# Performance work log

Measured on AMD Instinct MI355X. Metric: run time of the kernel, lower is better.

The kernel has to match this reference:

```python
import jax, jax.numpy as jnp
import numpy as np

N_NODES = 100000
N_EDGES = 1000000
N_QUERY = 100000
F_IN = 64
HIDDEN = 64
LABEL_DIM = 2


def setup_inputs() -> dict:
    key = jax.random.key(0)
    ks = jax.random.split(key, 16)
    inp = {}
    for i, nm in enumerate(["Xr", "Xi", "Xj", "Xk"]):
        inp[nm] = jax.random.normal(ks[i], (N_NODES, F_IN), dtype=jnp.float32)
    for i, nm in enumerate(["norm_r", "norm_i", "norm_j", "norm_k"]):
        inp[nm] = jax.random.normal(ks[4 + i], (N_EDGES,), dtype=jnp.float32) * 0.1
    inp["edge_index"] = jax.random.randint(ks[8], (2, N_EDGES), 0, N_NODES)
    inp["query_edges"] = jax.random.randint(ks[9], (N_QUERY, 2), 0, N_NODES)
    s1 = (2.0 / (F_IN + HIDDEN)) ** 0.5  # glorot
    inp["W1"] = jax.random.normal(ks[10], (4, F_IN, HIDDEN), dtype=jnp.float32) * s1
    inp["b1"] = jnp.zeros((4, HIDDEN), dtype=jnp.float32)
    s2 = (2.0 / (HIDDEN + HIDDEN)) ** 0.5
    inp["W2"] = jax.random.normal(ks[11], (4, HIDDEN, HIDDEN), dtype=jnp.float32) * s2
    inp["b2"] = jnp.zeros((4, HIDDEN), dtype=jnp.float32)
    inp["Cw"] = jax.random.normal(ks[12], (LABEL_DIM, 8 * HIDDEN), dtype=jnp.float32) * 0.05
    inp["Cb"] = jnp.zeros((LABEL_DIM,), dtype=jnp.float32)
    return inp


def _quaconv(Xs, src, dst, norms, W, b, n_nodes):
    # Xs: list of 4 [N,F] components; norms: list of 4 [E] Laplacian norms.
    # P[a][b] = propagate(X_a, -norm_b) = scatter_add over dst of (-norm_b)_e * X_a[src_e]
    P = []
    for a in range(4):
        G = Xs[a][src]  # [E, F] gather, reused for all 4 norms
        P.append([jax.ops.segment_sum((-norms[b])[:, None] * G, dst, num_segments=n_nodes)
                  for b in range(4)])
    Tr = P[0][0] - P[1][1] - P[2][2] - P[3][3]
    Ti = P[1][0] + P[0][1] + P[3][2] - P[2][3]
    Tj = P[2][0] - P[3][1] + P[0][2] + P[1][3]
    Tk = P[3][0] + P[2][1] - P[1][2] + P[0][3]
    Wr, Wi, Wj, Wk = W[0], W[1], W[2], W[3]
    out_r = Tr @ Wr - Ti @ Wi - Tj @ Wj - Tk @ Wk + b[0]
    out_i = Tr @ Wi + Ti @ Wr + Tj @ Wk - Tk @ Wj + b[1]
    out_j = Tr @ Wj - Ti @ Wk + Tj @ Wr + Tk @ Wi + b[2]
    out_k = Tr @ Wk + Ti @ Wj - Tj @ Wi + Tk @ Wr + b[3]
    return out_r, out_i, out_j, out_k


def _forward(Xr, Xi, Xj, Xk, norm_r, norm_i, norm_j, norm_k,
             W1, b1, W2, b2, Cw, Cb, edge_index, query_edges):
    src, dst = edge_index[0], edge_index[1]
    n = Xr.shape[0]
    norms = [norm_r, norm_i, norm_j, norm_k]
    Xs = [Xr, Xi, Xj, Xk]
    for W, b in ((W1, b1), (W2, b2)):
        Xs = list(_quaconv(Xs, src, dst, norms, W, b, n))
        # complex_relu_layer_different: mask = 1.0*(x>=0); mask*x == relu(x)
        Xs = [jax.nn.relu(x) for x in Xs]
    q0, q1 = query_edges[:, 0], query_edges[:, 1]
    # cat(real[q0], real[q1], imag_i[q0], imag_i[q1], ...) -> [Eq, 8*hidden]
    feats = jnp.concatenate([c[idx] for c in Xs for idx in (q0, q1)], axis=-1)
    # dropout is identity at inference; Conv1d(kernel=1) == linear over channels
    logits = feats @ Cw.T + Cb  # [Eq, label_dim]
    return jax.nn.log_softmax(logits, axis=-1)


def reference(Xr, Xi, Xj, Xk, norm_r, norm_i, norm_j, norm_k,
              W1, b1, W2, b2, Cw, Cb, edge_index, query_edges):
    return _forward(Xr, Xi, Xj, Xk, norm_r, norm_i, norm_j, norm_k,
                    W1, b1, W2, b2, Cw, Cb, edge_index, query_edges)
```

## Files before the change

kernel.cpp:

```cpp
#include <hip/hip_runtime.h>
#include <hip/hip_bf16.h>

#define N_NODESC 100000
#define N_EDGESC 1000000
#define N_QUERYC 100000

typedef short short8 __attribute__((ext_vector_type(8)));
typedef short s16x2 __attribute__((ext_vector_type(2)));
typedef float f32x4 __attribute__((ext_vector_type(4)));

__device__ __forceinline__ float ldf(const void* p, int i, int isbf) {
  return isbf ? __bfloat162float(((const __hip_bfloat16*)p)[i])
              : ((const float*)p)[i];
}
__device__ __forceinline__ unsigned short f2b(float x) {
  __hip_bfloat16 h = __float2bfloat16(x);
  return *(unsigned short*)&h;
}
__device__ __forceinline__ s16x2 u2s(unsigned u) {
  union { unsigned u; s16x2 s; } c; c.u = u; return c.s;
}
__device__ __forceinline__ void gload16(const void* g, void* l) {
  __builtin_amdgcn_global_load_lds(
      (const __attribute__((address_space(1))) void*)g,
      (__attribute__((address_space(3))) void*)l, 16, 0, 0);
}

__global__ __launch_bounds__(256) void k_setup(
    const void* x, int* flag, int* cnt, int n,
    const void* W1, const void* b1, const void* W2, const void* b2,
    unsigned short* __restrict__ Wq1, float* __restrict__ bcat1,
    unsigned short* __restrict__ Wq2, float* __restrict__ bcat2, int nzBlocks) {
  int bid = blockIdx.x;
  int t = threadIdx.x;
  if (bid < nzBlocks) {
    int i = bid * 256 + t;
    if (i < n) cnt[i] = 0;
    return;
  }
  __shared__ int scnt;
  if (t == 0) scnt = 0;
  __syncthreads();
  const unsigned short* h = (const unsigned short*)x;
  int local = 0;
  for (int i = t; i < 4096; i += 256) {
    int e = (h[i] >> 7) & 0xFF;
    if (e >= 107 && e <= 133) local++;
  }
  atomicAdd(&scnt, local);
  __syncthreads();
  int isbf = (scnt >= 3482) ? 1 : 0;
  if (bid == nzBlocks) {
    if (t == 0) *flag = isbf;
    return;
  }
  int wb = bid - nzBlocks - 1;
  int layer = wb >> 6;
  const void* W = layer ? W2 : W1;
  const void* b = layer ? b2 : b1;
  unsigned short* Wq = layer ? Wq2 : Wq1;
  float* bcat = layer ? bcat2 : bcat1;
  int tt = (wb & 63) * 256 + t;
  int w4 = tt >> 12;
  int hh = (tt >> 6) & 63;
  int kk = tt & 63;
  int s = (kk >> 3) ^ (hh & 7);
  Wq[(w4 * 64 + hh) * 64 + s * 8 + (kk & 7)] = f2b(ldf(W, w4 * 4096 + kk * 64 + hh, isbf));
  if (tt < 256) bcat[tt] = ldf(b, tt, isbf);
}

__global__ __launch_bounds__(256) void k_fill0_ilv(
    const int* __restrict__ ei,
    const void* nr, const void* ni, const void* nj, const void* nk,
    int* __restrict__ cnt, uint4* __restrict__ temp, int ne, int fillBlocks,
    const void* X0, const void* X1, const void* X2, const void* X3,
    const int* __restrict__ flagp, unsigned short* __restrict__ Xg, int n) {
  int bid = blockIdx.x;
  if (bid < fillBlocks) {
    int isbf = *flagp;
    int e = bid * 256 + threadIdx.x;
    if (e >= ne) return;
    int s = ei[e];
    int d = ei[ne + e];
    int pos = atomicAdd(&cnt[d], 1);
    uint4 r;
    r.x = (unsigned)s;
    r.y = (unsigned)f2b(-ldf(nr, e, isbf)) | ((unsigned)f2b(-ldf(ni, e, isbf)) << 16);
    r.z = (unsigned)f2b(-ldf(nj, e, isbf)) | ((unsigned)f2b(-ldf(nk, e, isbf)) << 16);
    r.w = (unsigned)pos;
    temp[e] = r;
  } else {
    int isbf = *flagp;
    int lane = threadIdx.x & 63;
    int node = (bid - fillBlocks) * 4 + (threadIdx.x >> 6);
    if (node >= n) return;
    int idx = node * 64 + lane;
    unsigned int lo = f2b(ldf(X0, idx, isbf)) | ((unsigned int)f2b(ldf(X1, idx, isbf)) << 16);
    unsigned int hi = f2b(ldf(X2, idx, isbf)) | ((unsigned int)f2b(ldf(X3, idx, isbf)) << 16);
    uint2 g = make_uint2(lo, hi);
    *(uint2*)(Xg + (size_t)node * 256 + lane * 4) = g;
  }
}

__global__ void k_scan1(const int* __restrict__ cnt, int* __restrict__ off,
                        int* __restrict__ partials, int n) {
  __shared__ int s[1024];
  int t = threadIdx.x;
  int idx = blockIdx.x * 1024 + t;
  int v = (idx < n) ? cnt[idx] : 0;
  s[t] = v;
  __syncthreads();
  for (int d = 1; d < 1024; d <<= 1) {
    int tmp = (t >= d) ? s[t - d] : 0;
    __syncthreads();
    s[t] += tmp;
    __syncthreads();
  }
  if (idx < n) off[idx] = s[t] - v;
  if (t == 1023) partials[blockIdx.x] = s[1023];
}

__global__ void k_scan2(const int* __restrict__ partials, int* __restrict__ pref,
                        int* __restrict__ off, int nb, int npos) {
  __shared__ int s[128];
  int t = threadIdx.x;
  int v = (t < nb) ? partials[t] : 0;
  s[t] = v;
  __syncthreads();
  for (int d = 1; d < 128; d <<= 1) {
    int tmp = (t >= d) ? s[t - d] : 0;
    __syncthreads();
    s[t] += tmp;
    __syncthreads();
  }
  if (t < nb) pref[t] = s[t] - v;
  if (t == 127) off[npos] = s[127];
}

__global__ void k_scan3(int* __restrict__ off, const int* __restrict__ pref, int n) {
  int i = blockIdx.x * 256 + threadIdx.x;
  if (i < n) off[i] = off[i] + pref[i >> 10];
}

__global__ void k_scatter(const int* __restrict__ ei, const uint4* __restrict__ temp,
                          const int* __restrict__ off, uint4* __restrict__ recs, int ne) {
  int e = blockIdx.x * 256 + threadIdx.x;
  if (e >= ne) return;
  uint4 r = temp[e];
  int d = ei[ne + e];
  int pos = (int)r.w;
  recs[off[d] + pos] = r;
}

#if __has_builtin(__builtin_amdgcn_fdot2_f32_bf16)
#define USE_DOT2 1
#else
#define USE_DOT2 0
#endif
__global__ __launch_bounds__(128, 8) void k_agg(
    const unsigned short* __restrict__ Xg, const int* __restrict__ off,
    const uint4* __restrict__ recs, unsigned short* __restrict__ Tf, int nnodes) {
  __shared__ unsigned short tl4[2][4][256];
  int lane = threadIdx.x & 63;
  int w = threadIdx.x >> 6;
  int gq = blockIdx.x * 2 + w;
  int n0 = gq * 4;
  if (n0 >= nnodes) return;

  int o_[5];
#pragma unroll
  for (int i = 0; i < 5; i++) o_[i] = __builtin_amdgcn_readfirstlane(off[n0 + i]);

#pragma unroll
  for (int n = 0; n < 4; ++n) {
    int rs = o_[n], re = o_[n + 1];
    float tr = 0.f, ti = 0.f, tj = 0.f, tk = 0.f;

    auto qacc = [&](uint2 g, unsigned mx, unsigned my) {
#if USE_DOT2
      unsigned a = mx, b = my;
      unsigned sa = (a >> 16) | (a << 16);
      unsigned sb = (b >> 16) | (b << 16);
      unsigned A1 = a ^ 0x80000000u;
      unsigned A2 = b ^ 0x80008000u;
      unsigned B2 = sb ^ 0x00008000u;
      unsigned D2 = sb ^ 0x80000000u;
      s16x2 gx = u2s(g.x), gy = u2s(g.y);
      tr = __builtin_amdgcn_fdot2_f32_bf16(u2s(A1), gx, tr, false);
      tr = __builtin_amdgcn_fdot2_f32_bf16(u2s(A2), gy, tr, false);
      ti = __builtin_amdgcn_fdot2_f32_bf16(u2s(sa), gx, ti, false);
      ti = __builtin_amdgcn_fdot2_f32_bf16(u2s(B2), gy, ti, false);
      tj = __builtin_amdgcn_fdot2_f32_bf16(u2s(b),  gx, tj, false);
      tj = __builtin_amdgcn_fdot2_f32_bf16(u2s(A1), gy, tj, false);
      tk = __builtin_amdgcn_fdot2_f32_bf16(u2s(D2), gx, tk, false);
      tk = __builtin_amdgcn_fdot2_f32_bf16(u2s(sa), gy, tk, false);
#else
      float mr = __uint_as_float(mx << 16), mi = __uint_as_float(mx & 0xffff0000u);
      float mj = __uint_as_float(my << 16), mk = __uint_as_float(my & 0xffff0000u);
      float xr = __uint_as_float(g.x << 16), xi = __uint_as_float(g.x & 0xffff0000u);
      float xj = __uint_as_float(g.y << 16), xk = __uint_as_float(g.y & 0xffff0000u);
      tr += mr * xr - mi * xi - mj * xj - mk * xk;
      ti += mr * xi + mi * xr + mj * xk - mk * xj;
      tj += mr * xj - mi * xk + mj * xr + mk * xi;
      tk += mr * xk + mi * xj - mj * xi + mk * xr;
#endif
    };

    int e = rs;
    for (; e + 8 <= re; e += 8) {
      uint4 r[8];
#pragma unroll
      for (int u = 0; u < 8; u++) r[u] = recs[e + u];
      int ss[8];
      unsigned sx[8], sy[8];
#pragma unroll
      for (int u = 0; u < 8; u++) {
        ss[u] = __builtin_amdgcn_readfirstlane((int)r[u].x);
        sx[u] = __builtin_amdgcn_readfirstlane(r[u].y);
        sy[u] = __builtin_amdgcn_readfirstlane(r[u].z);
      }
      uint2 g[8];
#pragma unroll
      for (int u = 0; u < 8; u++)
        g[u] = *(const uint2*)(Xg + (size_t)ss[u] * 256 + lane * 4);
#pragma unroll
      for (int u = 0; u < 8; u++) qacc(g[u], sx[u], sy[u]);
    }
    for (; e < re; ++e) {
      uint4 r = recs[e];
      int s = __builtin_amdgcn_readfirstlane((int)r.x);
      unsigned mx = __builtin_amdgcn_readfirstlane(r.y);
      unsigned my = __builtin_amdgcn_readfirstlane(r.z);
      uint2 g0 = *(const uint2*)(Xg + (size_t)s * 256 + lane * 4);
      qacc(g0, mx, my);
    }

    tl4[w][n][lane] = f2b(tr);
    tl4[w][n][64 + lane] = f2b(ti);
    tl4[w][n][128 + lane] = f2b(tj);
    tl4[w][n][192 + lane] = f2b(tk);
  }
  __builtin_amdgcn_wave_barrier();

  size_t blk = (size_t)(gq >> 2) * 4096;
  int qi = gq & 3;
#pragma unroll
  for (int h = 0; h < 2; ++h) {
    int m = h * 64 + lane;
    int n = m & 3, l = m >> 2;
    uint4 v = *(const uint4*)&tl4[w][n][l * 8];
    size_t o = blk + (size_t)(l >> 2) * 512 + (l & 3) * 128 + qi * 32 + n * 8;
    *(uint4*)(Tf + o) = v;
  }
}

__global__ __launch_bounds__(256, 2) void k_gemm(
    const unsigned short* __restrict__ A, const unsigned short* __restrict__ Wq,
    const float* __restrict__ bias, int M, int mode,
    unsigned short* __restrict__ XgOut,
    float* __restrict__ P, const void* Cw, const int* __restrict__ flagp) {
  __shared__ unsigned short Wsm[16384];

  int t = threadIdx.x;
  int lane = t & 63;
  int w = t >> 6;
  int l15 = lane & 15, quad = lane >> 4;
  int m0 = blockIdx.x * 64;
  int hh = (w & 1) * 32;

#pragma unroll
  for (int i = 0; i < 8; i++)
    gload16((const char*)Wq + (size_t)(i * 256 + t) * 16,
            (char*)Wsm + (size_t)(i * 256 + w * 64) * 16);
  __syncthreads();

  short8 av[2][8];
  int n16 = blockIdx.x * 4 + (w >> 1) * 2;
#pragma unroll
  for (int mi = 0; mi < 2; mi++)
#pragma unroll
    for (int kc = 0; kc < 8; kc++)
      av[mi][kc] = *(const short8*)(A + (size_t)(n16 + mi) * 4096 + kc * 512 + lane * 8);

  f32x4 acc[2][4][2];
#pragma unroll
  for (int mi = 0; mi < 2; mi++)
#pragma unroll
    for (int c = 0; c < 4; c++)
#pragma unroll
      for (int hb = 0; hb < 2; hb++) acc[mi][c][hb] = (f32x4){0.f, 0.f, 0.f, 0.f};

#pragma unroll
  for (int kc = 0; kc < 8; kc++) {
    int a = kc >> 1;
    short8 bv[4][2];
#pragma unroll
    for (int c = 0; c < 4; c++) {
      int w4 = a ^ c;
      int neg = (0x3950 >> (a * 4 + c)) & 1;
#pragma unroll
      for (int hb = 0; hb < 2; hb++) {
        int h = hh + hb * 16 + l15;
        int lc = ((kc & 1) * 4 + quad) ^ (l15 & 7);
        short8 bb = *(const short8*)&Wsm[(w4 * 64 + h) * 64 + lc * 8];
        if (neg) {
          uint4 u = *(uint4*)&bb;
          u.x ^= 0x80008000u; u.y ^= 0x80008000u;
          u.z ^= 0x80008000u; u.w ^= 0x80008000u;
          bb = *(short8*)&u;
        }
        bv[c][hb] = bb;
      }
    }
#pragma unroll
    for (int mi = 0; mi < 2; mi++)
#pragma unroll
      for (int c = 0; c < 4; c++)
#pragma unroll
        for (int hb = 0; hb < 2; hb++)
          acc[mi][c][hb] =
              __builtin_amdgcn_mfma_f32_16x16x32_bf16(av[mi][kc], bv[c][hb], acc[mi][c][hb], 0, 0, 0);
  }

  float bias_v[4][2];
#pragma unroll
  for (int c = 0; c < 4; c++)
#pragma unroll
    for (int hb = 0; hb < 2; hb++) bias_v[c][hb] = bias[c * 64 + hh + hb * 16 + l15];

  if (mode == 0) {
#pragma unroll
    for (int mi = 0; mi < 2; mi++) {
#pragma unroll
      for (int hb = 0; hb < 2; hb++) {
#pragma unroll
        for (int r = 0; r < 4; r++) {
          int node = m0 + (w >> 1) * 32 + mi * 16 + quad * 4 + r;
          unsigned int lo =
              f2b(fmaxf(acc[mi][0][hb][r] + bias_v[0][hb], 0.f)) |
              ((unsigned int)f2b(fmaxf(acc[mi][1][hb][r] + bias_v[1][hb], 0.f)) << 16);
          unsigned int hi =
              f2b(fmaxf(acc[mi][2][hb][r] + bias_v[2][hb], 0.f)) |
              ((unsigned int)f2b(fmaxf(acc[mi][3][hb][r] + bias_v[3][hb], 0.f)) << 16);
          *(uint2*)(XgOut + (size_t)node * 256 + (hh + hb * 16 + l15) * 4) =
              make_uint2(lo, hi);
        }
      }
    }
  } else {
    int isbf = *flagp;
    float cw[4][2][4];
#pragma unroll
    for (int c = 0; c < 4; c++)
#pragma unroll
      for (int hb = 0; hb < 2; hb++) {
        int h = hh + hb * 16 + l15;
#pragma unroll
        for (int d = 0; d < 2; d++)
#pragma unroll
          for (int e = 0; e < 2; e++)
            cw[c][hb][e + 2 * d] = ldf(Cw, d * 512 + c * 128 + e * 64 + h, isbf);
      }
    float* Pout = P + ((hh == 0) ? 0 : 4);
#pragma unroll
    for (int mi = 0; mi < 2; mi++) {
#pragma unroll
      for (int r = 0; r < 4; r++) {
        int node = m0 + (w >> 1) * 32 + mi * 16 + quad * 4 + r;
        float pd0 = 0.f, pd1 = 0.f, pd2 = 0.f, pd3 = 0.f;
#pragma unroll
        for (int c = 0; c < 4; c++)
#pragma unroll
          for (int hb = 0; hb < 2; hb++) {
            float v = fmaxf(acc[mi][c][hb][r] + bias_v[c][hb], 0.f);
            pd0 += v * cw[c][hb][0];
            pd1 += v * cw[c][hb][1];
            pd2 += v * cw[c][hb][2];
            pd3 += v * cw[c][hb][3];
          }
#pragma unroll
        for (int o = 1; o < 16; o <<= 1) {
          pd0 += __shfl_xor(pd0, o);
          pd1 += __shfl_xor(pd1, o);
          pd2 += __shfl_xor(pd2, o);
          pd3 += __shfl_xor(pd3, o);
        }
        if (l15 == 0 && node < M) {
          f32x4 st = {pd0, pd1, pd2, pd3};
          *(f32x4*)(Pout + (size_t)node * 8) = st;
        }
      }
    }
  }
}

__global__ void k_query(const int* __restrict__ qe, const float* __restrict__ P,
                        const void* Cb, const int* __restrict__ flagp,
                        void* out, int nq) {
  int isbf = *flagp;
  int q = blockIdx.x * 256 + threadIdx.x;
  if (q >= nq) return;
  int q0 = qe[q * 2], q1 = qe[q * 2 + 1];
  f32x4 a0 = *(const f32x4*)(P + (size_t)q0 * 8);
  f32x4 b0 = *(const f32x4*)(P + (size_t)q0 * 8 + 4);
  f32x4 a1 = *(const f32x4*)(P + (size_t)q1 * 8);
  f32x4 b1 = *(const f32x4*)(P + (size_t)q1 * 8 + 4);
  float l0 = (a0[0] + b0[0]) + (a1[1] + b1[1]) + ldf(Cb, 0, isbf);
  float l1 = (a0[2] + b0[2]) + (a1[3] + b1[3]) + ldf(Cb, 1, isbf);
  float m = fmaxf(l0, l1);
  float lse = m + logf(expf(l0 - m) + expf(l1 - m));
  float o0 = l0 - lse, o1 = l1 - lse;
  if (isbf) {
    __hip_bfloat16* o = (__hip_bfloat16*)out;
    o[q * 2] = __float2bfloat16(o0);
    o[q * 2 + 1] = __float2bfloat16(o1);
  } else {
    float* o = (float*)out;
    o[q * 2] = o0;
    o[q * 2 + 1] = o1;
  }
}

extern "C" void kernel_launch(void* const* d_in, const int* in_sizes, int n_in,
                              void* d_out, int out_size, void* d_ws, size_t ws_size,
                              hipStream_t stream) {
  const int N = N_NODESC, NE = N_EDGESC, NQ = N_QUERYC;
  const int NPAD = 100224;

  char* w = (char*)d_ws;
  auto alloc = [&](size_t bytes) -> void* {
    void* p = (void*)w;
    w += (bytes + 255) & ~(size_t)255;
    return p;
  };
  int* flag       = (int*)alloc(4);
  int* offsets    = (int*)alloc((size_t)(N + 1) * 4);
  int* cnt        = (int*)alloc((size_t)N * 4);
  int* partials   = (int*)alloc(128 * 4);
  int* pref       = (int*)alloc(128 * 4);
  uint4* recs     = (uint4*)alloc((size_t)NE * 16);
  unsigned short* Tf = (unsigned short*)alloc((size_t)NPAD * 256 * 2);
  unsigned short* Xg = (unsigned short*)alloc((size_t)NPAD * 256 * 2);
  unsigned short* Wq1 = (unsigned short*)alloc(16384 * 2);
  unsigned short* Wq2 = (unsigned short*)alloc(16384 * 2);
  float* bcat1    = (float*)alloc(256 * 4);
  float* bcat2    = (float*)alloc(256 * 4);
  float* P        = (float*)alloc((size_t)N * 8 * 4);
  uint4* temp     = (uint4*)Tf;
  (void)ws_size; (void)n_in; (void)in_sizes; (void)out_size;

  const int* ei = (const int*)d_in[8];

  int nzBlocks = (N + 255) / 256;
  k_setup<<<nzBlocks + 1 + 128, 256, 0, stream>>>(
      d_in[0], flag, cnt, N,
      d_in[10], d_in[11], d_in[12], d_in[13],
      Wq1, bcat1, Wq2, bcat2, nzBlocks);

  int fillBlocks = (NE + 255) / 256;
  int ilvBlocks = (N + 3) / 4;
  k_fill0_ilv<<<fillBlocks + ilvBlocks, 256, 0, stream>>>(
      ei, d_in[4], d_in[5], d_in[6], d_in[7], cnt, temp, NE, fillBlocks,
      d_in[0], d_in[1], d_in[2], d_in[3], flag, Xg, N);

  k_scan1<<<(N + 1023) / 1024, 1024, 0, stream>>>(cnt, offsets, partials, N);
  k_scan2<<<1, 128, 0, stream>>>(partials, pref, offsets, (N + 1023) / 1024, N);
  k_scan3<<<(N + 255) / 256, 256, 0, stream>>>(offsets, pref, N);
  k_scatter<<<fillBlocks, 256, 0, stream>>>(ei, temp, offsets, recs, NE);

  int ggrid = (N + 63) / 64;
  int nquads = (N + 3) / 4;
  int agrid = (nquads + 1) / 2;

  k_agg<<<agrid, 128, 0, stream>>>(Xg, offsets, recs, Tf, N);
  k_gemm<<<ggrid, 256, 0, stream>>>(Tf, Wq1, bcat1, N, 0, Xg, nullptr, nullptr, flag);

  k_agg<<<agrid, 128, 0, stream>>>(Xg, offsets, recs, Tf, N);
  k_gemm<<<ggrid, 256, 0, stream>>>(Tf, Wq2, bcat2, N, 1, nullptr, P, d_in[14], flag);

  k_query<<<(NQ + 255) / 256, 256, 0, stream>>>((const int*)d_in[9], P, d_in[15],
                                                flag, d_out, NQ);
}
```

Before: 462.5 us.

## Fuse neighbor aggregation with quaternion GEMM and merge scan passes

Combines the edge aggregation kernel and the MFMA GEMM kernel into one kernel per layer. Each 512-thread block aggregates 64 nodes into swizzled LDS and then runs the MFMA directly from LDS, so the intermediate T buffer no longer goes to global memory and back. Weights are now read from global memory and no longer staged in LDS. The two small scan kernels are also merged into one that recomputes chunk prefixes per block. The cost is that larger blocks have to wait at a barrier for their slowest aggregation wave, and occupancy changes.

Result: slower. 754.8 us (+63.2%).

```diff
diff --git a/kernel.cpp b/kernel.cpp
--- a/kernel.cpp
+++ b/kernel.cpp
@@ -19,11 +19,6 @@
 }
 __device__ __forceinline__ s16x2 u2s(unsigned u) {
   union { unsigned u; s16x2 s; } c; c.u = u; return c.s;
-}
-__device__ __forceinline__ void gload16(const void* g, void* l) {
-  __builtin_amdgcn_global_load_lds(
-      (const __attribute__((address_space(1))) void*)g,
-      (__attribute__((address_space(3))) void*)l, 16, 0, 0);
 }
 
 __global__ __launch_bounds__(256) void k_setup(
@@ -120,26 +115,24 @@
   if (t == 1023) partials[blockIdx.x] = s[1023];
 }
 
-__global__ void k_scan2(const int* __restrict__ partials, int* __restrict__ pref,
-                        int* __restrict__ off, int nb, int npos) {
-  __shared__ int s[128];
+__global__ __launch_bounds__(256) void k_scan3f(int* __restrict__ off,
+                                                const int* __restrict__ partials,
+                                                int n, int nchunks) {
+  __shared__ int sp[256];
   int t = threadIdx.x;
-  int v = (t < nb) ? partials[t] : 0;
-  s[t] = v;
+  sp[t] = (t < nchunks) ? partials[t] : 0;
   __syncthreads();
-  for (int d = 1; d < 128; d <<= 1) {
-    int tmp = (t >= d) ? s[t - d] : 0;
+  for (int d = 1; d < 256; d <<= 1) {
+    int tmp = (t >= d) ? sp[t - d] : 0;
     __syncthreads();
-    s[t] += tmp;
+    sp[t] += tmp;
     __syncthreads();
   }
-  if (t < nb) pref[t] = s[t] - v;
-  if (t == 127) off[npos] = s[127];
-}
-
-__global__ void k_scan3(int* __restrict__ off, const int* __restrict__ pref, int n) {
-  int i = blockIdx.x * 256 + threadIdx.x;
-  if (i < n) off[i] = off[i] + pref[i >> 10];
+  int chunk = blockIdx.x >> 2;
+  int pref = (chunk == 0) ? 0 : sp[chunk - 1];
+  int i = blockIdx.x * 256 + t;
+  if (i < n) off[i] += pref;
+  if (blockIdx.x == gridDim.x - 1 && t == 255) off[n] = sp[255];
 }
 
 __global__ void k_scatter(const int* __restrict__ ei, const uint4* __restrict__ temp,
@@ -157,31 +150,35 @@
 #else
 #define USE_DOT2 0
 #endif
-__global__ __launch_bounds__(128, 8) void k_agg(
-    const unsigned short* __restrict__ Xg, const int* __restrict__ off,
-    const uint4* __restrict__ recs, unsigned short* __restrict__ Tf, int nnodes) {
-  __shared__ unsigned short tl4[2][4][256];
-  int lane = threadIdx.x & 63;
-  int w = threadIdx.x >> 6;
-  int gq = blockIdx.x * 2 + w;
-  int n0 = gq * 4;
-  if (n0 >= nnodes) return;
-
-  int o_[5];
-#pragma unroll
-  for (int i = 0; i < 5; i++) o_[i] = __builtin_amdgcn_readfirstlane(off[n0 + i]);
-
-#pragma unroll
-  for (int n = 0; n < 4; ++n) {
-    int rs = o_[n], re = o_[n + 1];
+__global__ __launch_bounds__(512, 6) void k_aggemm(
+    const unsigned short* __restrict__ XgIn, const int* __restrict__ off,
+    const uint4* __restrict__ recs, const unsigned short* __restrict__ Wq,
+    const float* __restrict__ bias, int M, int mode,
+    unsigned short* __restrict__ XgOut, float* __restrict__ P,
+    const void* Cw, const int* __restrict__ flagp, int nnodes) {
+  __shared__ unsigned short Tsm[16384];
+  int tid = threadIdx.x;
+  int lane = tid & 63;
+  int w = tid >> 6;
+  int base = blockIdx.x * 64;
+  int first = base + w * 8;
+  bool act = (first < nnodes);
+
+  int o_[9];
+  if (act) {
+#pragma unroll
+    for (int i = 0; i < 9; i++) o_[i] = __builtin_amdgcn_readfirstlane(off[first + i]);
+  }
+
+  for (int a = 0; a < 8; ++a) {
     float tr = 0.f, ti = 0.f, tj = 0.f, tk = 0.f;
 
     auto qacc = [&](uint2 g, unsigned mx, unsigned my) {
 #if USE_DOT2
-      unsigned a = mx, b = my;
-      unsigned sa = (a >> 16) | (a << 16);
+      unsigned aa = mx, b = my;
+      unsigned sa = (aa >> 16) | (aa << 16);
       unsigned sb = (b >> 16) | (b << 16);
-      unsigned A1 = a ^ 0x80000000u;
+      unsigned A1 = aa ^ 0x80000000u;
       unsigned A2 = b ^ 0x80008000u;
       unsigned B2 = sb ^ 0x00008000u;
       unsigned D2 = sb ^ 0x80000000u;
@@ -206,120 +203,84 @@
 #endif
     };
 
-    int e = rs;
-    for (; e + 8 <= re; e += 8) {
-      uint4 r[8];
-#pragma unroll
-      for (int u = 0; u < 8; u++) r[u] = recs[e + u];
-      int ss[8];
-      unsigned sx[8], sy[8];
-#pragma unroll
-      for (int u = 0; u < 8; u++) {
-        ss[u] = __builtin_amdgcn_readfirstlane((int)r[u].x);
-        sx[u] = __builtin_amdgcn_readfirstlane(r[u].y);
-        sy[u] = __builtin_amdgcn_readfirstlane(r[u].z);
-      }
-      uint2 g[8];
-#pragma unroll
-      for (int u = 0; u < 8; u++)
-        g[u] = *(const uint2*)(Xg + (size_t)ss[u] * 256 + lane * 4);
-#pragma unroll
-      for (int u = 0; u < 8; u++) qacc(g[u], sx[u], sy[u]);
+    if (act) {
+      int rs = o_[a], re = o_[a + 1];
+      int e = rs;
+      for (; e + 8 <= re; e += 8) {
+        uint4 r[8];
+#pragma unroll
+        for (int u = 0; u < 8; u++) r[u] = recs[e + u];
+        int ss[8];
+        unsigned sx[8], sy[8];
+#pragma unroll
+        for (int u = 0; u < 8; u++) {
+          ss[u] = __builtin_amdgcn_readfirstlane((int)r[u].x);
+          sx[u] = __builtin_amdgcn_readfirstlane(r[u].y);
+          sy[u] = __builtin_amdgcn_readfirstlane(r[u].z);
+        }
+        uint2 g[8];
+#pragma unroll
+        for (int u = 0; u < 8; u++)
+          g[u] = *(const uint2*)(XgIn + (size_t)ss[u] * 256 + lane * 4);
+#pragma unroll
+        for (int u = 0; u < 8; u++) qacc(g[u], sx[u], sy[u]);
+      }
+      for (; e < re; ++e) {
+        uint4 r = recs[e];
+        int s = __builtin_amdgcn_readfirstlane((int)r.x);
+        unsigned mx = __builtin_amdgcn_readfirstlane(r.y);
+        unsigned my = __builtin_amdgcn_readfirstlane(r.z);
+        uint2 g0 = *(const uint2*)(XgIn + (size_t)s * 256 + lane * 4);
+        qacc(g0, mx, my);
+      }
     }
-    for (; e < re; ++e) {
-      uint4 r = recs[e];
-      int s = __builtin_amdgcn_readfirstlane((int)r.x);
-      unsigned mx = __builtin_amdgcn_readfirstlane(r.y);
-      unsigned my = __builtin_amdgcn_readfirstlane(r.z);
-      uint2 g0 = *(const uint2*)(Xg + (size_t)s * 256 + lane * 4);
-      qacc(g0, mx, my);
-    }
-
-    tl4[w][n][lane] = f2b(tr);
-    tl4[w][n][64 + lane] = f2b(ti);
-    tl4[w][n][128 + lane] = f2b(tj);
-    tl4[w][n][192 + lane] = f2b(tk);
-  }
-  __builtin_amdgcn_wave_barrier();
-
-  size_t blk = (size_t)(gq >> 2) * 4096;
-  int qi = gq & 3;
-#pragma unroll
-  for (int h = 0; h < 2; ++h) {
-    int m = h * 64 + lane;
-    int n = m & 3, l = m >> 2;
-    uint4 v = *(const uint4*)&tl4[w][n][l * 8];
-    size_t o = blk + (size_t)(l >> 2) * 512 + (l & 3) * 128 + qi * 32 + n * 8;
-    *(uint4*)(Tf + o) = v;
-  }
-}
-
-__global__ __launch_bounds__(256, 2) void k_gemm(
-    const unsigned short* __restrict__ A, const unsigned short* __restrict__ Wq,
-    const float* __restrict__ bias, int M, int mode,
-    unsigned short* __restrict__ XgOut,
-    float* __restrict__ P, const void* Cw, const int* __restrict__ flagp) {
-  __shared__ unsigned short Wsm[16384];
-
-  int t = threadIdx.x;
-  int lane = t & 63;
-  int w = t >> 6;
+
+    int nl = w * 8 + a;
+    unsigned sw = (unsigned)((nl & 7) << 4);
+    char* tb = (char*)Tsm + nl * 512;
+    *(unsigned short*)(tb + (((unsigned)(lane * 2)) ^ sw)) = f2b(tr);
+    *(unsigned short*)(tb + (((unsigned)(128 + lane * 2)) ^ sw)) = f2b(ti);
+    *(unsigned short*)(tb + (((unsigned)(256 + lane * 2)) ^ sw)) = f2b(tj);
+    *(unsigned short*)(tb + (((unsigned)(384 + lane * 2)) ^ sw)) = f2b(tk);
+  }
+  __syncthreads();
+
   int l15 = lane & 15, quad = lane >> 4;
-  int m0 = blockIdx.x * 64;
+  int g16 = w >> 1;
   int hh = (w & 1) * 32;
 
-#pragma unroll
-  for (int i = 0; i < 8; i++)
-    gload16((const char*)Wq + (size_t)(i * 256 + t) * 16,
-            (char*)Wsm + (size_t)(i * 256 + w * 64) * 16);
-  __syncthreads();
-
-  short8 av[2][8];
-  int n16 = blockIdx.x * 4 + (w >> 1) * 2;
-#pragma unroll
-  for (int mi = 0; mi < 2; mi++)
-#pragma unroll
-    for (int kc = 0; kc < 8; kc++)
-      av[mi][kc] = *(const short8*)(A + (size_t)(n16 + mi) * 4096 + kc * 512 + lane * 8);
-
-  f32x4 acc[2][4][2];
-#pragma unroll
-  for (int mi = 0; mi < 2; mi++)
-#pragma unroll
-    for (int c = 0; c < 4; c++)
-#pragma unroll
-      for (int hb = 0; hb < 2; hb++) acc[mi][c][hb] = (f32x4){0.f, 0.f, 0.f, 0.f};
-
+  f32x4 acc[4][2];
+#pragma unroll
+  for (int c = 0; c < 4; c++)
+#pragma unroll
+    for (int hb = 0; hb < 2; hb++) acc[c][hb] = (f32x4){0.f, 0.f, 0.f, 0.f};
+
+  int nlr = g16 * 16 + l15;
+  unsigned swr = (unsigned)((nlr & 7) << 4);
 #pragma unroll
   for (int kc = 0; kc < 8; kc++) {
-    int a = kc >> 1;
-    short8 bv[4][2];
+    short8 av = *(const short8*)((const char*)Tsm +
+                 (((unsigned)(nlr * 512 + kc * 64 + quad * 16)) ^ swr));
+    int a2 = kc >> 1;
 #pragma unroll
     for (int c = 0; c < 4; c++) {
-      int w4 = a ^ c;
-      int neg = (0x3950 >> (a * 4 + c)) & 1;
+      int w4 = a2 ^ c;
+      int neg = (0x3950 >> (a2 * 4 + c)) & 1;
 #pragma unroll
       for (int hb = 0; hb < 2; hb++) {
         int h = hh + hb * 16 + l15;
         int lc = ((kc & 1) * 4 + quad) ^ (l15 & 7);
-        short8 bb = *(const short8*)&Wsm[(w4 * 64 + h) * 64 + lc * 8];
+        short8 bb = *(const short8*)&Wq[(w4 * 64 + h) * 64 + lc * 8];
         if (neg) {
           uint4 u = *(uint4*)&bb;
           u.x ^= 0x80008000u; u.y ^= 0x80008000u;
           u.z ^= 0x80008000u; u.w ^= 0x80008000u;
           bb = *(short8*)&u;
         }
-        bv[c][hb] = bb;
+        acc[c][hb] =
+            __builtin_amdgcn_mfma_f32_16x16x32_bf16(av, bb, acc[c][hb], 0, 0, 0);
       }
     }
-#pragma unroll
-    for (int mi = 0; mi < 2; mi++)
-#pragma unroll
-      for (int c = 0; c < 4; c++)
-#pragma unroll
-        for (int hb = 0; hb < 2; hb++)
-          acc[mi][c][hb] =
-              __builtin_amdgcn_mfma_f32_16x16x32_bf16(av[mi][kc], bv[c][hb], acc[mi][c][hb], 0, 0, 0);
   }
 
   float bias_v[4][2];
@@ -330,21 +291,18 @@
 
   if (mode == 0) {
 #pragma unroll
-    for (int mi = 0; mi < 2; mi++) {
-#pragma unroll
-      for (int hb = 0; hb < 2; hb++) {
-#pragma unroll
-        for (int r = 0; r < 4; r++) {
-          int node = m0 + (w >> 1) * 32 + mi * 16 + quad * 4 + r;
-          unsigned int lo =
-              f2b(fmaxf(acc[mi][0][hb][r] + bias_v[0][hb], 0.f)) |
-              ((unsigned int)f2b(fmaxf(acc[mi][1][hb][r] + bias_v[1][hb], 0.f)) << 16);
-          unsigned int hi =
-              f2b(fmaxf(acc[mi][2][hb][r] + bias_v[2][hb], 0.f)) |
-              ((unsigned int)f2b(fmaxf(acc[mi][3][hb][r] + bias_v[3][hb], 0.f)) << 16);
-          *(uint2*)(XgOut + (size_t)node * 256 + (hh + hb * 16 + l15) * 4) =
-              make_uint2(lo, hi);
-        }
+    for (int hb = 0; hb < 2; hb++) {
+#pragma unroll
+      for (int r = 0; r < 4; r++) {
+        int node = base + g16 * 16 + quad * 4 + r;
+        unsigned int lo =
+            f2b(fmaxf(acc[0][hb][r] + bias_v[0][hb], 0.f)) |
+            ((unsigned int)f2b(fmaxf(acc[1][hb][r] + bias_v[1][hb], 0.f)) << 16);
+        unsigned int hi =
+            f2b(fmaxf(acc[2][hb][r] + bias_v[2][hb], 0.f)) |
+            ((unsigned int)f2b(fmaxf(acc[3][hb][r] + bias_v[3][hb], 0.f)) << 16);
+        *(uint2*)(XgOut + (size_t)node * 256 + (hh + hb * 16 + l15) * 4) =
+            make_uint2(lo, hi);
       }
     }
   } else {
@@ -363,32 +321,29 @@
       }
     float* Pout = P + ((hh == 0) ? 0 : 4);
 #pragma unroll
-    for (int mi = 0; mi < 2; mi++) {
-#pragma unroll
-      for (int r = 0; r < 4; r++) {
-        int node = m0 + (w >> 1) * 32 + mi * 16 + quad * 4 + r;
-        float pd0 = 0.f, pd1 = 0.f, pd2 = 0.f, pd3 = 0.f;
-#pragma unroll
-        for (int c = 0; c < 4; c++)
-#pragma unroll
-          for (int hb = 0; hb < 2; hb++) {
-            float v = fmaxf(acc[mi][c][hb][r] + bias_v[c][hb], 0.f);
-            pd0 += v * cw[c][hb][0];
-            pd1 += v * cw[c][hb][1];
-            pd2 += v * cw[c][hb][2];
-            pd3 += v * cw[c][hb][3];
-          }
-#pragma unroll
-        for (int o = 1; o < 16; o <<= 1) {
-          pd0 += __shfl_xor(pd0, o);
-          pd1 += __shfl_xor(pd1, o);
-          pd2 += __shfl_xor(pd2, o);
-          pd3 += __shfl_xor(pd3, o);
+    for (int r = 0; r < 4; r++) {
+      int node = base + g16 * 16 + quad * 4 + r;
+      float pd0 = 0.f, pd1 = 0.f, pd2 = 0.f, pd3 = 0.f;
+#pragma unroll
+      for (int c = 0; c < 4; c++)
+#pragma unroll
+        for (int hb = 0; hb < 2; hb++) {
+          float v = fmaxf(acc[c][hb][r] + bias_v[c][hb], 0.f);
+          pd0 += v * cw[c][hb][0];
+          pd1 += v * cw[c][hb][1];
+          pd2 += v * cw[c][hb][2];
+          pd3 += v * cw[c][hb][3];
         }
-        if (l15 == 0 && node < M) {
-          f32x4 st = {pd0, pd1, pd2, pd3};
-          *(f32x4*)(Pout + (size_t)node * 8) = st;
-        }
+#pragma unroll
+      for (int o = 1; o < 16; o <<= 1) {
+        pd0 += __shfl_xor(pd0, o);
+        pd1 += __shfl_xor(pd1, o);
+        pd2 += __shfl_xor(pd2, o);
+        pd3 += __shfl_xor(pd3, o);
+      }
+      if (l15 == 0 && node < M) {
+        f32x4 st = {pd0, pd1, pd2, pd3};
+        *(f32x4*)(Pout + (size_t)node * 8) = st;
       }
     }
   }
@@ -437,16 +392,15 @@
   int* offsets    = (int*)alloc((size_t)(N + 1) * 4);
   int* cnt        = (int*)alloc((size_t)N * 4);
   int* partials   = (int*)alloc(128 * 4);
-  int* pref       = (int*)alloc(128 * 4);
   uint4* recs     = (uint4*)alloc((size_t)NE * 16);
-  unsigned short* Tf = (unsigned short*)alloc((size_t)NPAD * 256 * 2);
-  unsigned short* Xg = (unsigned short*)alloc((size_t)NPAD * 256 * 2);
+  unsigned short* Xa = (unsigned short*)alloc((size_t)NPAD * 256 * 2);
+  unsigned short* Xb = (unsigned short*)alloc((size_t)NPAD * 256 * 2);
   unsigned short* Wq1 = (unsigned short*)alloc(16384 * 2);
   unsigned short* Wq2 = (unsigned short*)alloc(16384 * 2);
   float* bcat1    = (float*)alloc(256 * 4);
   float* bcat2    = (float*)alloc(256 * 4);
   float* P        = (float*)alloc((size_t)N * 8 * 4);
-  uint4* temp     = (uint4*)Tf;
+  uint4* temp     = (uint4*)Xb;
   (void)ws_size; (void)n_in; (void)in_sizes; (void)out_size;
 
   const int* ei = (const int*)d_in[8];
@@ -461,22 +415,19 @@
   int ilvBlocks = (N + 3) / 4;
   k_fill0_ilv<<<fillBlocks + ilvBlocks, 256, 0, stream>>>(
       ei, d_in[4], d_in[5], d_in[6], d_in[7], cnt, temp, NE, fillBlocks,
-      d_in[0], d_in[1], d_in[2], d_in[3], flag, Xg, N);
-
-  k_scan1<<<(N + 1023) / 1024, 1024, 0, stream>>>(cnt, offsets, partials, N);
-  k_scan2<<<1, 128, 0, stream>>>(partials, pref, offsets, (N + 1023) / 1024, N);
-  k_scan3<<<(N + 255) / 256, 256, 0, stream>>>(offsets, pref, N);
+      d_in[0], d_in[1], d_in[2], d_in[3], flag, Xa, N);
+
+  int nchunks = (N + 1023) / 1024;
+  k_scan1<<<nchunks, 1024, 0, stream>>>(cnt, offsets, partials, N);
+  k_scan3f<<<(N + 255) / 256, 256, 0, stream>>>(offsets, partials, N, nchunks);
   k_scatter<<<fillBlocks, 256, 0, stream>>>(ei, temp, offsets, recs, NE);
 
-  int ggrid = (N + 63) / 64;
-  int nquads = (N + 3) / 4;
-  int agrid = (nquads + 1) / 2;
-
-  k_agg<<<agrid, 128, 0, stream>>>(Xg, offsets, recs, Tf, N);
-  k_gemm<<<ggrid, 256, 0, stream>>>(Tf, Wq1, bcat1, N, 0, Xg, nullptr, nullptr, flag);
-
-  k_agg<<<agrid, 128, 0, stream>>>(Xg, offsets, recs, Tf, N);
-  k_gemm<<<ggrid, 256, 0, stream>>>(Tf, Wq2, bcat2, N, 1, nullptr, P, d_in[14], flag);
+  int nb = (N + 63) / 64;
+
+  k_aggemm<<<nb, 512, 0, stream>>>(Xa, offsets, recs, Wq1, bcat1, N, 0,
+                                   Xb, nullptr, nullptr, flag, N);
+  k_aggemm<<<nb, 512, 0, stream>>>(Xb, offsets, recs, Wq2, bcat2, N, 1,
+                                   nullptr, P, d_in[14], flag, N);
 
   k_query<<<(NQ + 255) / 256, 256, 0, stream>>>((const int*)d_in[9], P, d_in[15],
                                                 flag, d_out, NQ);
```
